# Kernel optimization log

Hardware: AMD Instinct MI355X
Metric: run time of the kernel (lower is better)

The kernel has to match this reference:

```python
import jax, jax.numpy as jnp
import numpy as np

N, E, G = 50000, 500000, 2048
IN_ATOM, IN_BOND, H, OUT = 128, 16, 256, 2


def setup_inputs() -> dict:
    key = jax.random.key(0)
    ks = iter(jax.random.split(key, 64))
    nrm = lambda shape, s=0.05: jax.random.normal(next(ks), shape, dtype=jnp.float32) * s
    inp = {}
    inp["x"] = nrm((N, IN_ATOM), 1.0)
    inp["edge_attr"] = nrm((E, IN_BOND), 1.0)
    inp["edge_index"] = jax.random.randint(next(ks), (2, E), 0, N)
    inp["batch"] = jnp.sort(jax.random.randint(next(ks), (N,), 0, G))
    dims = [IN_ATOM, H, H]  # input width of each GINE layer
    for i, d in enumerate(dims):
        inp[f"l{i}_We"] = nrm((IN_BOND, d))            # GINEConv edge lin
        inp[f"l{i}_be"] = jnp.zeros((d,), jnp.float32)
        inp[f"l{i}_W1"] = nrm((d, H))                  # mlp Linear 1
        inp[f"l{i}_b1"] = jnp.zeros((H,), jnp.float32)
        inp[f"l{i}_W2"] = nrm((H, H))                  # mlp Linear 2
        inp[f"l{i}_b2"] = jnp.zeros((H,), jnp.float32)
        inp[f"l{i}_eps"] = jnp.zeros((1,), jnp.float32)  # train_eps scalar
    # Bayesian head: weight = mu + exp(log_sigma) * noise
    inp["h1_wmu"] = nrm((H, H)); inp["h1_wls"] = jnp.full((H, H), -3.0, jnp.float32)
    inp["h1_bmu"] = jnp.zeros((H,), jnp.float32); inp["h1_bls"] = jnp.full((H,), -3.0, jnp.float32)
    inp["h2_wmu"] = nrm((H, OUT)); inp["h2_wls"] = jnp.full((H, OUT), -3.0, jnp.float32)
    inp["h2_bmu"] = jnp.zeros((OUT,), jnp.float32); inp["h2_bls"] = jnp.full((OUT,), -3.0, jnp.float32)
    inp["eps_w1"] = nrm((H, H), 1.0); inp["eps_b1"] = nrm((H,), 1.0)
    inp["eps_w2"] = nrm((H, OUT), 1.0); inp["eps_b2"] = nrm((OUT,), 1.0)
    return inp


def _gine_layer(h, src, dst, edge_attr, We, be, W1, b1, W2, b2, eps):
    e = edge_attr @ We + be                       # [E, d] edge projection
    m = jax.nn.relu(h[src] + e)                   # messages from source nodes
    agg = jax.ops.segment_sum(m, dst, num_segments=N)
    z = (1.0 + eps[0]) * h + agg
    z = jax.nn.relu(z @ W1 + b1) @ W2 + b2        # GINE mlp
    return jax.nn.relu(z)                          # backbone activation


def reference(x, edge_attr,
              l0_We, l0_be, l0_W1, l0_b1, l0_W2, l0_b2, l0_eps,
              l1_We, l1_be, l1_W1, l1_b1, l1_W2, l1_b2, l1_eps,
              l2_We, l2_be, l2_W1, l2_b1, l2_W2, l2_b2, l2_eps,
              h1_wmu, h1_wls, h1_bmu, h1_bls,
              h2_wmu, h2_wls, h2_bmu, h2_bls,
              eps_w1, eps_b1, eps_w2, eps_b2,
              edge_index, batch):
    src, dst = edge_index[0], edge_index[1]
    h = x
    layers = [
        (l0_We, l0_be, l0_W1, l0_b1, l0_W2, l0_b2, l0_eps),
        (l1_We, l1_be, l1_W1, l1_b1, l1_W2, l1_b2, l1_eps),
        (l2_We, l2_be, l2_W1, l2_b1, l2_W2, l2_b2, l2_eps),
    ]
    for (We, be, W1, b1, W2, b2, eps) in layers:
        h = _gine_layer(h, src, dst, edge_attr, We, be, W1, b1, W2, b2, eps)
    hg = jax.ops.segment_sum(h, batch, num_segments=G)  # global_add_pool -> [G, H]
    # Bayesian head (dropout is identity at eval)
    w1 = h1_wmu + jnp.exp(h1_wls) * eps_w1
    b1 = h1_bmu + jnp.exp(h1_bls) * eps_b1
    h1 = jax.nn.silu(hg @ w1 + b1)
    w2 = h2_wmu + jnp.exp(h2_wls) * eps_w2
    b2 = h2_bmu + jnp.exp(h2_bls) * eps_b2
    return h1 @ w2 + b2  # [G, OUT]
```

## Files before the change

### kernel.cpp

```cpp
#include <hip/hip_runtime.h>
#include <hip/hip_bf16.h>
#include <math.h>


#define THREADS 256

typedef __attribute__((ext_vector_type(8))) short bf16x8;
typedef __attribute__((ext_vector_type(4))) float f32x4;

__device__ __forceinline__ unsigned short f2bf(float x) {
    __hip_bfloat16 h = __float2bfloat16(x);
    return __builtin_bit_cast(unsigned short, h);
}
__device__ __forceinline__ float bflo(unsigned u) {
    return __builtin_bit_cast(float, u << 16);
}
__device__ __forceinline__ float bfhi(unsigned u) {
    return __builtin_bit_cast(float, u & 0xffff0000u);
}
__device__ __forceinline__ float bf2f(unsigned short u) {
    return __builtin_bit_cast(float, (unsigned)u << 16);
}
__device__ __forceinline__ unsigned pk(float a, float b) {
    return (unsigned)f2bf(a) | ((unsigned)f2bf(b) << 16);
}

__global__ __launch_bounds__(THREADS) void hist_kernel(
    const int* __restrict__ ei, int* __restrict__ deg, int E)
{
    int e = blockIdx.x * THREADS + threadIdx.x;
    if (e < E) atomicAdd(&deg[ei[E + e]], 1);
}

__global__ __launch_bounds__(1024) void scan_kernel(
    const int* __restrict__ deg, int* __restrict__ rowptr, int n)
{
    __shared__ int wsum[16];
    __shared__ int carry_s;
    const int t    = threadIdx.x;
    const int lane = t & 63, wv = t >> 6;
    if (t == 0) carry_s = 0;
    __syncthreads();
    for (int base = 0; base < n; base += 1024) {
        int i = base + t;
        int incl = (i < n) ? deg[i] : 0;
#pragma unroll
        for (int off = 1; off < 64; off <<= 1) {
            int u = __shfl_up(incl, off, 64);
            if (lane >= off) incl += u;
        }
        if (lane == 63) wsum[wv] = incl;
        __syncthreads();
        if (wv == 0) {
            int s = (lane < 16) ? wsum[lane] : 0;
#pragma unroll
            for (int off = 1; off < 16; off <<= 1) {
                int u = __shfl_up(s, off, 64);
                if (lane >= off) s += u;
            }
            if (lane < 16) wsum[lane] = s;
        }
        __syncthreads();
        int waveoff = (wv == 0) ? 0 : wsum[wv - 1];
        int carry   = carry_s;
        if (i < n) rowptr[i + 1] = carry + waveoff + incl;
        __syncthreads();
        if (t == 1023) carry_s = carry + wsum[15];
        __syncthreads();
    }
    if (t == 0) rowptr[0] = 0;
}

__global__ __launch_bounds__(THREADS) void fill_kernel(
    const int* __restrict__ ei, const int* __restrict__ rowptr,
    int* __restrict__ cursor, int* __restrict__ csr_src,
    int* __restrict__ csr_dst, const float* __restrict__ edge_attr,
    unsigned short* __restrict__ ea16, int E)
{
    int e = blockIdx.x * THREADS + threadIdx.x;
    if (e >= E) return;
    int s = ei[e], d = ei[E + e];
    int pos  = atomicAdd(&cursor[d], 1);
    int slot = rowptr[d] + pos;
    csr_src[slot] = s;
    csr_dst[slot] = d;
    const float4* a = (const float4*)(edge_attr + (size_t)e * 16);
    float4 a0 = a[0], a1 = a[1], a2 = a[2], a3 = a[3];
    uint4* dst = (uint4*)(ea16 + (size_t)slot * 16);
    dst[0] = make_uint4(pk(a0.x, a0.y), pk(a0.z, a0.w), pk(a1.x, a1.y), pk(a1.z, a1.w));
    dst[1] = make_uint4(pk(a2.x, a2.y), pk(a2.z, a2.w), pk(a3.x, a3.y), pk(a3.z, a3.w));
}

__global__ __launch_bounds__(THREADS) void xprep_kernel(
    const float* __restrict__ x, unsigned short* __restrict__ xbf, int n4)
{
    int i = blockIdx.x * THREADS + threadIdx.x;
    if (i >= n4) return;
    float4 v = ((const float4*)x)[i];
    uint2 p;
    p.x = pk(v.x, v.y);
    p.y = pk(v.z, v.w);
    ((uint2*)xbf)[i] = p;
}

__global__ __launch_bounds__(THREADS) void wetrans_kernel(
    const float* __restrict__ We, unsigned short* __restrict__ Wtp, int D)
{
    int f = blockIdx.x * THREADS + threadIdx.x;
    if (f >= D) return;
#pragma unroll
    for (int k = 0; k < 16; k++) Wtp[f * 32 + k] = f2bf(We[k * D + f]);
#pragma unroll
    for (int k = 16; k < 32; k++) Wtp[f * 32 + k] = 0;
}

template<int D>
__global__ __launch_bounds__(THREADS) void edge_agg_kernel(
    const unsigned short* __restrict__ hbf,
    const unsigned short* __restrict__ ea16,
    const int* __restrict__ csr_src,
    const int* __restrict__ csr_dst,
    const unsigned short* __restrict__ Wtp,
    const float* __restrict__ be,
    unsigned short* __restrict__ agg,
    int E)
{
    constexpr int EPB = (D == 128) ? 64 : 32;
    constexpr int LDF = D + 8;
    __shared__ unsigned short msg[EPB * LDF];
    __shared__ int src_s[EPB];
    __shared__ int dst_x[EPB + 2];

    const int t    = threadIdx.x;
    const int e0   = blockIdx.x * EPB;
    const int lane = t & 63, wid = t >> 6;
    const int l15  = lane & 15, lgr = lane >> 4;

    for (int i = t; i < EPB; i += THREADS) {
        int e = e0 + i;
        src_s[i] = (e < E) ? csr_src[e] : 0;
    }
    for (int i = t; i < EPB + 2; i += THREADS) {
        int e = e0 + i - 1;
        dst_x[i] = (e < 0) ? -2 : ((e < E) ? csr_dst[e] : -1);
    }

    const int fb = (D == 128) ? (wid & 1) * 64 : wid * 64;
    const int eb = (D == 128) ? (wid >> 1) * 32 : 0;

    bf16x8 af[4];
#pragma unroll
    for (int mf = 0; mf < 4; mf++)
        af[mf] = *(const bf16x8*)(Wtp + (size_t)(fb + mf * 16 + l15) * 32 + lgr * 8);

    f32x4 acc[4][2];
#pragma unroll
    for (int mf = 0; mf < 4; mf++) {
        int fpos = fb + mf * 16 + lgr * 4;
        float4 bv4 = *(const float4*)(be + fpos);
        f32x4 binit = (f32x4){bv4.x, bv4.y, bv4.z, bv4.w};
        acc[mf][0] = binit;
        acc[mf][1] = binit;
    }

#pragma unroll
    for (int nf = 0; nf < 2; nf++) {
        int er = e0 + eb + nf * 16 + l15;
        bf16x8 bv = (bf16x8){0, 0, 0, 0, 0, 0, 0, 0};
        if (lgr < 2 && er < E)
            bv = *(const bf16x8*)(ea16 + (size_t)er * 16 + lgr * 8);
#pragma unroll
        for (int mf = 0; mf < 4; mf++)
            acc[mf][nf] = __builtin_amdgcn_mfma_f32_16x16x32_bf16(
                af[mf], bv, acc[mf][nf], 0, 0, 0);
    }

#pragma unroll
    for (int nf = 0; nf < 2; nf++) {
        int edge = eb + nf * 16 + l15;
#pragma unroll
        for (int mf = 0; mf < 4; mf++) {
            int fpos = fb + mf * 16 + lgr * 4;
            f32x4 v = acc[mf][nf];
            uint2 p;
            p.x = pk(v[0], v[1]);
            p.y = pk(v[2], v[3]);
            *(uint2*)(&msg[edge * LDF + fpos]) = p;
        }
    }
    __syncthreads();

    constexpr int LPF = D / 2;
    const int f2   = (t & (LPF - 1)) * 2;
    const int win  = t / LPF;
    const int base = win * 16;

    unsigned hv[16];
#pragma unroll
    for (int i = 0; i < 16; i++) {
        int src = src_s[base + i];
        hv[i] = *(const unsigned*)(hbf + (size_t)src * D + f2);
    }

    float a0 = 0.f, a1 = 0.f;
    int  cur = dst_x[base + 1];
    bool rs  = (dst_x[base] != cur);

#pragma unroll
    for (int i = 0; i < 16; ++i) {
        int el = base + i;
        int d  = dst_x[el + 1];
        if (d != cur) {
            if (cur >= 0) {
                unsigned short* ap = agg + (size_t)cur * D + f2;
                unsigned v32 = pk(a0, a1);
                if (rs) {
                    *(unsigned*)ap = v32;
                } else {
                    asm volatile("global_atomic_pk_add_bf16 %0, %1, off"
                                 :: "v"(ap), "v"(v32) : "memory");
                }
            }
            a0 = 0.f; a1 = 0.f; rs = true; cur = d;
        }
        unsigned pv = *(const unsigned*)(&msg[el * LDF + f2]);
        a0 += fmaxf(bflo(hv[i]) + bflo(pv), 0.f);
        a1 += fmaxf(bfhi(hv[i]) + bfhi(pv), 0.f);
    }
    if (cur >= 0) {
        bool re = (dst_x[base + 17] != cur);
        unsigned short* ap = agg + (size_t)cur * D + f2;
        unsigned v32 = pk(a0, a1);
        if (rs && re) {
            *(unsigned*)ap = v32;
        } else {
            asm volatile("global_atomic_pk_add_bf16 %0, %1, off"
                         :: "v"(ap), "v"(v32) : "memory");
        }
    }
}

__global__ __launch_bounds__(THREADS) void wtrans_kernel(
    const float* __restrict__ W, unsigned short* __restrict__ Wt, int K)
{
    __shared__ float tile[32][33];
    const int kb = blockIdx.x * 32, nb = blockIdx.y * 32;
    const int tx = threadIdx.x & 31, ty = threadIdx.x >> 5;
#pragma unroll
    for (int i = ty; i < 32; i += 8)
        tile[i][tx] = W[(size_t)(kb + i) * 256 + nb + tx];
    __syncthreads();
#pragma unroll
    for (int i = ty; i < 32; i += 8)
        Wt[(size_t)(nb + i) * K + kb + tx] = f2bf(tile[tx][i]);
}

template<int KIN>
__global__ __launch_bounds__(THREADS) void fused_mlp_kernel(
    const unsigned short* __restrict__ hin,
    const unsigned short* __restrict__ agg,
    const unsigned short* __restrict__ Wt1,
    const float* __restrict__ b1,
    const unsigned short* __restrict__ Wt2,
    const float* __restrict__ b2,
    const float* __restrict__ epsp,
    unsigned short* __restrict__ out,
    int nrows)
{
    constexpr int LDR = 72;
    constexpr int LDT = 264;
    __shared__ short As[64 * LDR];
    __shared__ short Bs[256 * LDR];
    __shared__ short Tmp[64 * LDT];

    const int t    = threadIdx.x;
    const int lane = t & 63;
    const int wid  = t >> 6;
    const int l15  = lane & 15, lgr = lane >> 4;
    const int r0   = blockIdx.x * 64;

    const float scale = 1.0f + epsp[0];

    f32x4 acc[4][4];
#pragma unroll
    for (int nf = 0; nf < 4; nf++) {
        float bv = b1[wid * 64 + nf * 16 + l15];
#pragma unroll
        for (int mf = 0; mf < 4; mf++)
            acc[mf][nf] = (f32x4){bv, bv, bv, bv};
    }

    for (int k0 = 0; k0 < KIN; k0 += 64) {
#pragma unroll
        for (int c = 0; c < 2; c++) {
            int idx = t + c * THREADS;
            int r   = idx >> 3;
            int kq  = idx & 7;
            int row = r0 + r;
            uint4 o = make_uint4(0, 0, 0, 0);
            if (row < nrows) {
                size_t g = (size_t)row * KIN + k0 + kq * 8;
                uint4 hv = *(const uint4*)(hin + g);
                uint4 av = *(const uint4*)(agg + g);
                o.x = pk(scale * bflo(hv.x) + bflo(av.x),
                         scale * bfhi(hv.x) + bfhi(av.x));
                o.y = pk(scale * bflo(hv.y) + bflo(av.y),
                         scale * bfhi(hv.y) + bfhi(av.y));
                o.z = pk(scale * bflo(hv.z) + bflo(av.z),
                         scale * bfhi(hv.z) + bfhi(av.z));
                o.w = pk(scale * bflo(hv.w) + bflo(av.w),
                         scale * bfhi(hv.w) + bfhi(av.w));
            }
            *(uint4*)(&As[r * LDR + kq * 8]) = o;
        }
#pragma unroll
        for (int c = 0; c < 8; c++) {
            int idx = t + c * THREADS;
            int n   = idx >> 3;
            int kq  = idx & 7;
            uint4 w = *(const uint4*)(Wt1 + (size_t)n * KIN + k0 + kq * 8);
            *(uint4*)(&Bs[n * LDR + kq * 8]) = w;
        }
        __syncthreads();

#pragma unroll
        for (int ks = 0; ks < 2; ks++) {
            bf16x8 afr[4], bfr[4];
#pragma unroll
            for (int mf = 0; mf < 4; mf++)
                afr[mf] = *(const bf16x8*)(&As[(mf * 16 + l15) * LDR + ks * 32 + lgr * 8]);
#pragma unroll
            for (int nf = 0; nf < 4; nf++)
                bfr[nf] = *(const bf16x8*)(&Bs[(wid * 64 + nf * 16 + l15) * LDR + ks * 32 + lgr * 8]);
#pragma unroll
            for (int mf = 0; mf < 4; mf++)
#pragma unroll
                for (int nf = 0; nf < 4; nf++)
                    acc[mf][nf] = __builtin_amdgcn_mfma_f32_16x16x32_bf16(
                        afr[mf], bfr[nf], acc[mf][nf], 0, 0, 0);
        }
        __syncthreads();
    }

#pragma unroll
    for (int nf = 0; nf < 4; nf++) {
        int col = wid * 64 + nf * 16 + l15;
#pragma unroll
        for (int mf = 0; mf < 4; mf++) {
            f32x4 v = acc[mf][nf];
#pragma unroll
            for (int r = 0; r < 4; r++) {
                int row = mf * 16 + lgr * 4 + r;
                Tmp[row * LDT + col] = (short)f2bf(fmaxf(v[r], 0.f));
            }
        }
    }
#pragma unroll
    for (int nf = 0; nf < 4; nf++) {
        float bv = b2[wid * 64 + nf * 16 + l15];
#pragma unroll
        for (int mf = 0; mf < 4; mf++)
            acc[mf][nf] = (f32x4){bv, bv, bv, bv};
    }
    __syncthreads();

    for (int k0 = 0; k0 < 256; k0 += 64) {
#pragma unroll
        for (int c = 0; c < 8; c++) {
            int idx = t + c * THREADS;
            int n   = idx >> 3;
            int kq  = idx & 7;
            uint4 w = *(const uint4*)(Wt2 + (size_t)n * 256 + k0 + kq * 8);
            *(uint4*)(&Bs[n * LDR + kq * 8]) = w;
        }
        __syncthreads();

#pragma unroll
        for (int ks = 0; ks < 2; ks++) {
            bf16x8 afr[4], bfr[4];
#pragma unroll
            for (int mf = 0; mf < 4; mf++)
                afr[mf] = *(const bf16x8*)(&Tmp[(mf * 16 + l15) * LDT + k0 + ks * 32 + lgr * 8]);
#pragma unroll
            for (int nf = 0; nf < 4; nf++)
                bfr[nf] = *(const bf16x8*)(&Bs[(wid * 64 + nf * 16 + l15) * LDR + ks * 32 + lgr * 8]);
#pragma unroll
            for (int mf = 0; mf < 4; mf++)
#pragma unroll
                for (int nf = 0; nf < 4; nf++)
                    acc[mf][nf] = __builtin_amdgcn_mfma_f32_16x16x32_bf16(
                        afr[mf], bfr[nf], acc[mf][nf], 0, 0, 0);
        }
        __syncthreads();
    }

#pragma unroll
    for (int nf = 0; nf < 4; nf++) {
        int col = wid * 64 + nf * 16 + l15;
#pragma unroll
        for (int mf = 0; mf < 4; mf++) {
            f32x4 v = acc[mf][nf];
#pragma unroll
            for (int r = 0; r < 4; r++) {
                int row = r0 + mf * 16 + lgr * 4 + r;
                if (row < nrows)
                    out[(size_t)row * 256 + col] = f2bf(fmaxf(v[r], 0.f));
            }
        }
    }
}

__global__ __launch_bounds__(THREADS) void pool_kernel(
    const unsigned short* __restrict__ hbf,
    const int*   __restrict__ batch,
    float*       __restrict__ hg,
    int nnodes)
{
    constexpr int CH = 64;
    __shared__ int b_s[CH];
    const int t  = threadIdx.x;
    const int v0 = blockIdx.x * CH;
    int cnt = nnodes - v0;
    if (cnt > CH) cnt = CH;
    if (cnt <= 0) return;
    if (t < cnt) b_s[t] = batch[v0 + t];
    __syncthreads();

    int curb  = b_s[0];
    float acc = 0.f;
    for (int v = 0; v < cnt; v++) {
        int b = b_s[v];
        if (b != curb) {
            atomicAdd(&hg[(size_t)curb * 256 + t], acc);
            acc = 0.f; curb = b;
        }
        acc += bf2f(hbf[(size_t)(v0 + v) * 256 + t]);
    }
    atomicAdd(&hg[(size_t)curb * 256 + t], acc);
}

__global__ void wprep_kernel(const float* __restrict__ mu,
                             const float* __restrict__ ls,
                             const float* __restrict__ eps,
                             float* __restrict__ w, int n)
{
    int i = blockIdx.x * THREADS + threadIdx.x;
    if (i < n) w[i] = mu[i] + expf(ls[i]) * eps[i];
}

__global__ __launch_bounds__(THREADS) void head_kernel(
    const float* __restrict__ hg,
    const float* __restrict__ w1,
    const float* __restrict__ h1_bmu, const float* __restrict__ h1_bls,
    const float* __restrict__ eps_b1,
    const float* __restrict__ h2_wmu, const float* __restrict__ h2_wls,
    const float* __restrict__ eps_w2,
    const float* __restrict__ h2_bmu, const float* __restrict__ h2_bls,
    const float* __restrict__ eps_b2,
    float* __restrict__ out)
{
    __shared__ float x_s[256];
    __shared__ float red[256];
    const int t = threadIdx.x;
    const int g = blockIdx.x;

    x_s[t] = hg[(size_t)g * 256 + t];
    __syncthreads();

    float acc = h1_bmu[t] + expf(h1_bls[t]) * eps_b1[t];
    for (int kk = 0; kk < 256; kk++) acc += x_s[kk] * w1[kk * 256 + t];
    float h1v = acc / (1.f + expf(-acc));

    float w2a = h2_wmu[t * 2 + 0] + expf(h2_wls[t * 2 + 0]) * eps_w2[t * 2 + 0];
    float w2b = h2_wmu[t * 2 + 1] + expf(h2_wls[t * 2 + 1]) * eps_w2[t * 2 + 1];

    red[t] = h1v * w2a;
    __syncthreads();
    for (int s = 128; s > 0; s >>= 1) {
        if (t < s) red[t] += red[t + s];
        __syncthreads();
    }
    if (t == 0) out[(size_t)g * 2 + 0] = red[0] + h2_bmu[0] + expf(h2_bls[0]) * eps_b2[0];
    __syncthreads();

    red[t] = h1v * w2b;
    __syncthreads();
    for (int s = 128; s > 0; s >>= 1) {
        if (t < s) red[t] += red[t + s];
        __syncthreads();
    }
    if (t == 0) out[(size_t)g * 2 + 1] = red[0] + h2_bmu[1] + expf(h2_bls[1]) * eps_b2[1];
}

extern "C" void kernel_launch(void* const* d_in, const int* in_sizes, int n_in,
                              void* d_out, int out_size, void* d_ws, size_t ws_size,
                              hipStream_t stream)
{
    const float* x         = (const float*)d_in[0];
    const float* edge_attr = (const float*)d_in[1];
    const int*   ei        = (const int*)d_in[2];
    const int*   batch     = (const int*)d_in[3];

    const float* We[3]  = { (const float*)d_in[4],  (const float*)d_in[11], (const float*)d_in[18] };
    const float* be[3]  = { (const float*)d_in[5],  (const float*)d_in[12], (const float*)d_in[19] };
    const float* W1[3]  = { (const float*)d_in[6],  (const float*)d_in[13], (const float*)d_in[20] };
    const float* b1[3]  = { (const float*)d_in[7],  (const float*)d_in[14], (const float*)d_in[21] };
    const float* W2[3]  = { (const float*)d_in[8],  (const float*)d_in[15], (const float*)d_in[22] };
    const float* b2[3]  = { (const float*)d_in[9],  (const float*)d_in[16], (const float*)d_in[23] };
    const float* epsl[3]= { (const float*)d_in[10], (const float*)d_in[17], (const float*)d_in[24] };

    const float* h1_wmu = (const float*)d_in[25];
    const float* h1_wls = (const float*)d_in[26];
    const float* h1_bmu = (const float*)d_in[27];
    const float* h1_bls = (const float*)d_in[28];
    const float* h2_wmu = (const float*)d_in[29];
    const float* h2_wls = (const float*)d_in[30];
    const float* h2_bmu = (const float*)d_in[31];
    const float* h2_bls = (const float*)d_in[32];
    const float* eps_w1 = (const float*)d_in[33];
    const float* eps_b1 = (const float*)d_in[34];
    const float* eps_w2 = (const float*)d_in[35];
    const float* eps_b2 = (const float*)d_in[36];

    const int N = in_sizes[0] / 128;
    const int E = in_sizes[1] / 16;
    const int G = out_size / 2;

    uintptr_t p = (uintptr_t)d_ws;
    auto carve = [&](size_t bytes) -> void* {
        void* r = (void*)p;
        p = (p + bytes + 255) & ~(uintptr_t)255;
        return r;
    };
    float* hg      = (float*)carve((size_t)G * 256 * 4);
    float* w1buf   = (float*)carve(256 * 256 * 4);
    int*   rowptr  = (int*)carve((size_t)(N + 1) * 4);
    int*   cursor  = (int*)carve((size_t)N * 4);
    int*   csr_src = (int*)carve((size_t)E * 4);
    int*   csr_dst = (int*)carve((size_t)E * 4);
    unsigned short* aggbf = (unsigned short*)carve((size_t)N * 256 * 2);
    unsigned short* ea16  = (unsigned short*)carve((size_t)E * 16 * 2);
    unsigned short* hbf   = (unsigned short*)carve((size_t)N * 256 * 2);
    unsigned short* xbf   = (unsigned short*)carve((size_t)N * 128 * 2);
    unsigned short* wep[3];
    wep[0] = (unsigned short*)carve(128 * 32 * 2);
    wep[1] = (unsigned short*)carve(256 * 32 * 2);
    wep[2] = (unsigned short*)carve(256 * 32 * 2);
    unsigned short* wt1[3], *wt2[3];
    wt1[0] = (unsigned short*)carve(256 * 128 * 2);
    for (int l = 0; l < 3; l++) {
        if (l) wt1[l] = (unsigned short*)carve(256 * 256 * 2);
        wt2[l] = (unsigned short*)carve(256 * 256 * 2);
    }

    const int eblocks     = (E + THREADS - 1) / THREADS;
    const int pool_blocks = (N + 63) / 64;
    const int mlp_blocks  = (N + 63) / 64;

    float* out = (float*)d_out;

    hipMemsetAsync(cursor, 0, (size_t)N * sizeof(int), stream);
    hist_kernel<<<eblocks, THREADS, 0, stream>>>(ei, cursor, E);
    scan_kernel<<<1, 1024, 0, stream>>>(cursor, rowptr, N);
    hipMemsetAsync(cursor, 0, (size_t)N * sizeof(int), stream);
    fill_kernel<<<eblocks, THREADS, 0, stream>>>(
        ei, rowptr, cursor, csr_src, csr_dst, edge_attr, ea16, E);
    xprep_kernel<<<(N * 32 + THREADS - 1) / THREADS, THREADS, 0, stream>>>(x, xbf, N * 32);

    wetrans_kernel<<<1, 128, 0, stream>>>(We[0], wep[0], 128);
    wetrans_kernel<<<1, 256, 0, stream>>>(We[1], wep[1], 256);
    wetrans_kernel<<<1, 256, 0, stream>>>(We[2], wep[2], 256);
    wtrans_kernel<<<dim3(4, 8), THREADS, 0, stream>>>(W1[0], wt1[0], 128);
    wtrans_kernel<<<dim3(8, 8), THREADS, 0, stream>>>(W2[0], wt2[0], 256);
    for (int l = 1; l < 3; l++) {
        wtrans_kernel<<<dim3(8, 8), THREADS, 0, stream>>>(W1[l], wt1[l], 256);
        wtrans_kernel<<<dim3(8, 8), THREADS, 0, stream>>>(W2[l], wt2[l], 256);
    }

    hipMemsetAsync(aggbf, 0, (size_t)N * 128 * sizeof(unsigned short), stream);
    edge_agg_kernel<128><<<(E + 63) / 64, THREADS, 0, stream>>>(
        xbf, ea16, csr_src, csr_dst, wep[0], be[0], aggbf, E);
    fused_mlp_kernel<128><<<mlp_blocks, THREADS, 0, stream>>>(
        xbf, aggbf, wt1[0], b1[0], wt2[0], b2[0], epsl[0], hbf, N);

    for (int l = 1; l < 3; l++) {
        hipMemsetAsync(aggbf, 0, (size_t)N * 256 * sizeof(unsigned short), stream);
        edge_agg_kernel<256><<<(E + 31) / 32, THREADS, 0, stream>>>(
            hbf, ea16, csr_src, csr_dst, wep[l], be[l], aggbf, E);
        fused_mlp_kernel<256><<<mlp_blocks, THREADS, 0, stream>>>(
            hbf, aggbf, wt1[l], b1[l], wt2[l], b2[l], epsl[l], hbf, N);
    }

    hipMemsetAsync(hg, 0, (size_t)G * 256 * sizeof(float), stream);
    pool_kernel<<<pool_blocks, THREADS, 0, stream>>>(hbf, batch, hg, N);

    wprep_kernel<<<(256 * 256 + THREADS - 1) / THREADS, THREADS, 0, stream>>>(
        h1_wmu, h1_wls, eps_w1, w1buf, 256 * 256);
    head_kernel<<<G, THREADS, 0, stream>>>(
        hg, w1buf, h1_bmu, h1_bls, eps_b1,
        h2_wmu, h2_wls, eps_w2, h2_bmu, h2_bls, eps_b2, out);
}
```

Before: 448.8 us.

## Load MLP weights directly from global, vectorize scan, use 32-bit gather offsets

The fused MLP kernel no longer stages weight tiles in shared memory. Each wave now reads its B fragments straight from global (L2-resident) weights, which removes the large Bs buffer and several block barriers and may raise occupancy. The degree scan now handles four elements per thread with int4 loads, and the message kernel builds gather and scatter addresses from 32-bit unsigned offsets to save address arithmetic. The cost is uncoalesced, repeated global reads of the weights by every block.

```diff
diff --git a/kernel.cpp b/kernel.cpp
--- a/kernel.cpp
+++ b/kernel.cpp
@@ -41,9 +41,17 @@
     const int lane = t & 63, wv = t >> 6;
     if (t == 0) carry_s = 0;
     __syncthreads();
-    for (int base = 0; base < n; base += 1024) {
-        int i = base + t;
-        int incl = (i < n) ? deg[i] : 0;
+    for (int base = 0; base < n; base += 4096) {
+        int i = base + t * 4;
+        int4 v = make_int4(0, 0, 0, 0);
+        if (i + 3 < n)      v = *(const int4*)(deg + i);
+        else if (i < n) {
+            v.x = deg[i];
+            v.y = (i + 1 < n) ? deg[i + 1] : 0;
+            v.z = (i + 2 < n) ? deg[i + 2] : 0;
+        }
+        int p1 = v.x + v.y, p2 = p1 + v.z, tot = p2 + v.w;
+        int incl = tot;
 #pragma unroll
         for (int off = 1; off < 64; off <<= 1) {
             int u = __shfl_up(incl, off, 64);
@@ -62,10 +70,13 @@
         }
         __syncthreads();
         int waveoff = (wv == 0) ? 0 : wsum[wv - 1];
-        int carry   = carry_s;
-        if (i < n) rowptr[i + 1] = carry + waveoff + incl;
-        __syncthreads();
-        if (t == 1023) carry_s = carry + wsum[15];
+        int tbase   = carry_s + waveoff + incl - tot;
+        if (i     < n) rowptr[i + 1] = tbase + v.x;
+        if (i + 1 < n) rowptr[i + 2] = tbase + p1;
+        if (i + 2 < n) rowptr[i + 3] = tbase + p2;
+        if (i + 3 < n) rowptr[i + 4] = tbase + tot;
+        __syncthreads();
+        if (t == 1023) carry_s = carry_s + wsum[15];
         __syncthreads();
     }
     if (t == 0) rowptr[0] = 0;
@@ -151,7 +162,7 @@
     bf16x8 af[4];
 #pragma unroll
     for (int mf = 0; mf < 4; mf++)
-        af[mf] = *(const bf16x8*)(Wtp + (size_t)(fb + mf * 16 + l15) * 32 + lgr * 8);
+        af[mf] = *(const bf16x8*)(Wtp + (unsigned)(fb + mf * 16 + l15) * 32 + lgr * 8);
 
     f32x4 acc[4][2];
 #pragma unroll
@@ -198,8 +209,8 @@
     unsigned hv[16];
 #pragma unroll
     for (int i = 0; i < 16; i++) {
-        int src = src_s[base + i];
-        hv[i] = *(const unsigned*)(hbf + (size_t)src * D + f2);
+        unsigned off = (unsigned)src_s[base + i] * D + f2;
+        hv[i] = *(const unsigned*)(hbf + off);
     }
 
     float a0 = 0.f, a1 = 0.f;
@@ -212,7 +223,7 @@
         int d  = dst_x[el + 1];
         if (d != cur) {
             if (cur >= 0) {
-                unsigned short* ap = agg + (size_t)cur * D + f2;
+                unsigned short* ap = agg + ((unsigned)cur * D + f2);
                 unsigned v32 = pk(a0, a1);
                 if (rs) {
                     *(unsigned*)ap = v32;
@@ -229,7 +240,7 @@
     }
     if (cur >= 0) {
         bool re = (dst_x[base + 17] != cur);
-        unsigned short* ap = agg + (size_t)cur * D + f2;
+        unsigned short* ap = agg + ((unsigned)cur * D + f2);
         unsigned v32 = pk(a0, a1);
         if (rs && re) {
             *(unsigned*)ap = v32;
@@ -270,7 +281,6 @@
     constexpr int LDR = 72;
     constexpr int LDT = 264;
     __shared__ short As[64 * LDR];
-    __shared__ short Bs[256 * LDR];
     __shared__ short Tmp[64 * LDT];
 
     const int t    = threadIdx.x;
@@ -313,25 +323,18 @@
             }
             *(uint4*)(&As[r * LDR + kq * 8]) = o;
         }
-#pragma unroll
-        for (int c = 0; c < 8; c++) {
-            int idx = t + c * THREADS;
-            int n   = idx >> 3;
-            int kq  = idx & 7;
-            uint4 w = *(const uint4*)(Wt1 + (size_t)n * KIN + k0 + kq * 8);
-            *(uint4*)(&Bs[n * LDR + kq * 8]) = w;
-        }
         __syncthreads();
 
 #pragma unroll
         for (int ks = 0; ks < 2; ks++) {
             bf16x8 afr[4], bfr[4];
 #pragma unroll
+            for (int nf = 0; nf < 4; nf++)
+                bfr[nf] = *(const bf16x8*)(Wt1 +
+                    (size_t)(wid * 64 + nf * 16 + l15) * KIN + k0 + ks * 32 + lgr * 8);
+#pragma unroll
             for (int mf = 0; mf < 4; mf++)
                 afr[mf] = *(const bf16x8*)(&As[(mf * 16 + l15) * LDR + ks * 32 + lgr * 8]);
-#pragma unroll
-            for (int nf = 0; nf < 4; nf++)
-                bfr[nf] = *(const bf16x8*)(&Bs[(wid * 64 + nf * 16 + l15) * LDR + ks * 32 + lgr * 8]);
 #pragma unroll
             for (int mf = 0; mf < 4; mf++)
 #pragma unroll
@@ -364,26 +367,18 @@
     }
     __syncthreads();
 
+#pragma unroll
     for (int k0 = 0; k0 < 256; k0 += 64) {
-#pragma unroll
-        for (int c = 0; c < 8; c++) {
-            int idx = t + c * THREADS;
-            int n   = idx >> 3;
-            int kq  = idx & 7;
-            uint4 w = *(const uint4*)(Wt2 + (size_t)n * 256 + k0 + kq * 8);
-            *(uint4*)(&Bs[n * LDR + kq * 8]) = w;
-        }
-        __syncthreads();
-
 #pragma unroll
         for (int ks = 0; ks < 2; ks++) {
             bf16x8 afr[4], bfr[4];
 #pragma unroll
+            for (int nf = 0; nf < 4; nf++)
+                bfr[nf] = *(const bf16x8*)(Wt2 +
+                    (size_t)(wid * 64 + nf * 16 + l15) * 256 + k0 + ks * 32 + lgr * 8);
+#pragma unroll
             for (int mf = 0; mf < 4; mf++)
                 afr[mf] = *(const bf16x8*)(&Tmp[(mf * 16 + l15) * LDT + k0 + ks * 32 + lgr * 8]);
-#pragma unroll
-            for (int nf = 0; nf < 4; nf++)
-                bfr[nf] = *(const bf16x8*)(&Bs[(wid * 64 + nf * 16 + l15) * LDR + ks * 32 + lgr * 8]);
 #pragma unroll
             for (int mf = 0; mf < 4; mf++)
 #pragma unroll
@@ -391,7 +386,6 @@
                     acc[mf][nf] = __builtin_amdgcn_mfma_f32_16x16x32_bf16(
                         afr[mf], bfr[nf], acc[mf][nf], 0, 0, 0);
         }
-        __syncthreads();
     }
 
 #pragma unroll
```

Result: no change. 450.0 us (+0.3%).
